# Performance work log

Hardware: AMD Instinct MI355X
Metric: run time of the kernel (lower is better)

The kernel has to match this reference:

```python
import jax, jax.numpy as jnp
import numpy as np

B, S, D, H, L, V, FFM = 4, 2048, 512, 8, 6, 8000, 4
HD = D // H
FF = FFM * D


def setup_inputs() -> dict:
    key = jax.random.key(0)
    ks = jax.random.split(key, 12)
    sc = 0.02
    return {
        "tokens": jax.random.randint(ks[0], (B, S), 0, V),
        "embed": jax.random.normal(ks[1], (V, D), jnp.float32) * sc,
        "wq": jax.random.normal(ks[2], (L, D, D), jnp.float32) * sc,
        "wk": jax.random.normal(ks[3], (L, D, D), jnp.float32) * sc,
        "wv": jax.random.normal(ks[4], (L, D, D), jnp.float32) * sc,
        "wo": jax.random.normal(ks[5], (L, D, D), jnp.float32) * sc,
        "bo": jnp.zeros((L, D), jnp.float32),
        "w1": jax.random.normal(ks[6], (L, D, FF), jnp.float32) * sc,
        "b1": jnp.zeros((L, FF), jnp.float32),
        "w2": jax.random.normal(ks[7], (L, FF, D), jnp.float32) * sc,
        "b2": jnp.zeros((L, D), jnp.float32),
        "ln_g": jnp.ones((L, D), jnp.float32),
        "ln_b": jnp.zeros((L, D), jnp.float32),
        "lnf_g": jnp.ones((D,), jnp.float32),
        "lnf_b": jnp.zeros((D,), jnp.float32),
        "w_out": jax.random.normal(ks[8], (D, V), jnp.float32) * sc,
        "b_out": jnp.zeros((V,), jnp.float32),
    }


def _layernorm(x, g, b, eps=1e-5):
    m = jnp.mean(x, -1, keepdims=True)
    v = jnp.var(x, -1, keepdims=True)
    return (x - m) * jax.lax.rsqrt(v + eps) * g + b


def _pos_encoding():
    pos = jnp.arange(S, dtype=jnp.float32)[:, None]
    div = jnp.exp(jnp.arange(0, D, 2, dtype=jnp.float32) * (-np.log(10000.0) / D))
    pe = jnp.zeros((S, D), jnp.float32)
    pe = pe.at[:, 0::2].set(jnp.sin(pos * div))
    pe = pe.at[:, 1::2].set(jnp.cos(pos * div))
    return pe


def _forward(tokens, embed, wq, wk, wv, wo, bo, w1, b1, w2, b2, ln_g, ln_b,
             lnf_g, lnf_b, w_out, b_out):
    x = embed[tokens] + _pos_encoding()[None]  # [B,S,D]
    causal = jnp.tril(jnp.ones((S, S), bool))
    neg_inf = jnp.float32(-jnp.inf)
    # NOTE: original scales scores by 1/sqrt(n_embd) (key.weight.size(-1) == D)
    inv_scale = 1.0 / jnp.sqrt(jnp.float32(D))

    def block(x, p):
        pwq, pwk, pwv, pwo, pbo, pw1, pb1, pw2, pb2, g, b = p
        # attention sublayer (same LayerNorm params used for both sublayers,
        # matching the repo's reuse of add_and_norm_1)
        h = _layernorm(x, g, b)
        q = (h @ pwq).reshape(B, S, H, HD)
        k = (h @ pwk).reshape(B, S, H, HD)
        v = (h @ pwv).reshape(B, S, H, HD)
        scores = jnp.einsum('bqhd,bkhd->bhqk', q, k) * inv_scale
        scores = jnp.where(causal, scores, neg_inf)
        att = jax.nn.softmax(scores, axis=-1)
        o = jnp.einsum('bhqk,bkhd->bqhd', att, v).reshape(B, S, D)
        x = x + o @ pwo + pbo
        # FFN sublayer
        h2 = _layernorm(x, g, b)
        x = x + jax.nn.relu(h2 @ pw1 + pb1) @ pw2 + pb2
        return x, None

    params = (wq, wk, wv, wo, bo, w1, b1, w2, b2, ln_g, ln_b)
    x, _ = jax.lax.scan(block, x, params)
    x = _layernorm(x, lnf_g, lnf_b)
    logits = x @ w_out + b_out  # [B,S,V]
    return logits


def reference(tokens, embed, wq, wk, wv, wo, bo, w1, b1, w2, b2, ln_g, ln_b,
              lnf_g, lnf_b, w_out, b_out):
    return _forward(tokens, embed, wq, wk, wv, wo, bo, w1, b1, w2, b2,
                    ln_g, ln_b, lnf_g, lnf_b, w_out, b_out)
```

## Files before the change

kernel.cpp:

```cpp
#include <hip/hip_runtime.h>

#define Bsz 4
#define Ssz 2048
#define Dsz 512
#define Hsz 8
#define Lsz 6
#define Vsz 8000
#define FFsz 2048
#define Msz (Bsz*Ssz)
#define VszPad 8064

typedef unsigned short u16;
typedef unsigned int u32;
typedef __attribute__((ext_vector_type(8))) short bf16x8;
typedef __attribute__((ext_vector_type(4))) float f32x4;
typedef __attribute__((ext_vector_type(16))) float f32x16;
typedef __attribute__((ext_vector_type(4))) u32 u32x4;

__device__ __forceinline__ u16 f2b(float f) {
    union { float f; unsigned u; } x; x.f = f;
    return (u16)((x.u + 0x7fffu + ((x.u >> 16) & 1u)) >> 16);
}

#define GLOAD_LDS16(g, l) __builtin_amdgcn_global_load_lds( \
    (const __attribute__((address_space(1))) u32*)(g), \
    (__attribute__((address_space(3))) u32*)(l), 16, 0, 0)

__global__ __launch_bounds__(256) void embed_kernel(const int* __restrict__ tokens,
                                                    const float* __restrict__ embed,
                                                    float* __restrict__ x) {
    int idx = blockIdx.x * 256 + threadIdx.x;
    int row = idx >> 8, p = idx & 255;
    int tok = tokens[row];
    int s = row & (Ssz - 1);
    float div = __expf((float)p * (-9.210340371976184f / 256.f));
    float ang = (float)s * div;
    float2 e = ((const float2*)(embed + (size_t)tok * Dsz))[p];
    float2 o;
    o.x = e.x + sinf(ang);
    o.y = e.y + cosf(ang);
    ((float2*)(x + (size_t)row * Dsz))[p] = o;
}

__global__ __launch_bounds__(256) void ln_kernel(const float* __restrict__ x,
                                                 const float* __restrict__ g,
                                                 const float* __restrict__ bta,
                                                 u16* __restrict__ out) {
    int wave = threadIdx.x >> 6, lane = threadIdx.x & 63;
    int row = blockIdx.x * 4 + wave;
    const float4* xr = (const float4*)(x + (size_t)row * Dsz);
    float4 a = xr[lane * 2], c = xr[lane * 2 + 1];
    float vals[8] = {a.x, a.y, a.z, a.w, c.x, c.y, c.z, c.w};
    float s = 0.f;
    #pragma unroll
    for (int i = 0; i < 8; ++i) s += vals[i];
    #pragma unroll
    for (int o = 32; o; o >>= 1) s += __shfl_xor(s, o);
    float mean = s * (1.f / 512.f);
    float sq = 0.f;
    #pragma unroll
    for (int i = 0; i < 8; ++i) { float d = vals[i] - mean; sq += d * d; }
    #pragma unroll
    for (int o = 32; o; o >>= 1) sq += __shfl_xor(sq, o);
    float rstd = rsqrtf(sq * (1.f / 512.f) + 1e-5f);
    int base = lane * 8;
    bf16x8 rv;
    #pragma unroll
    for (int i = 0; i < 8; ++i)
        rv[i] = (short)f2b((vals[i] - mean) * rstd * g[base + i] + bta[base + i]);
    *(bf16x8*)(out + (size_t)row * Dsz + base) = rv;
}

__global__ __launch_bounds__(256) void tconv_kernel(const float* __restrict__ src,
                                                    u16* __restrict__ dst,
                                                    int R, int C,
                                                    size_t sstride, size_t dstride) {
    __shared__ float tile[32][33];
    const float* s = src + blockIdx.z * sstride;
    u16* d = dst + blockIdx.z * dstride;
    int c0 = blockIdx.x * 32, r0 = blockIdx.y * 32;
    int tx = threadIdx.x & 31, ty = threadIdx.x >> 5;
    #pragma unroll
    for (int i = 0; i < 32; i += 8)
        tile[ty + i][tx] = s[(size_t)(r0 + ty + i) * C + c0 + tx];
    __syncthreads();
    #pragma unroll
    for (int i = 0; i < 32; i += 8)
        d[(size_t)(c0 + ty + i) * R + r0 + tx] = f2b(tile[tx][ty + i]);
}

__global__ __launch_bounds__(256) void vtrans_kernel(const u16* __restrict__ qkv,
                                                     u16* __restrict__ vT) {
    __shared__ u16 tile[32][33];
    int bh = blockIdx.z, b = bh >> 3, hh = bh & 7;
    int s0 = blockIdx.x * 32, d0 = blockIdx.y * 32;
    int tx = threadIdx.x & 31, ty = threadIdx.x >> 5;
    #pragma unroll
    for (int i = 0; i < 32; i += 8)
        tile[ty + i][tx] = qkv[(size_t)(b * Ssz + s0 + ty + i) * 1536 + 1024 + hh * 64 + d0 + tx];
    __syncthreads();
    #pragma unroll
    for (int i = 0; i < 32; i += 8)
        vT[((size_t)bh * 64 + d0 + ty + i) * Ssz + s0 + tx] = tile[tx][ty + i];
}

template<bool BIAS, bool RES, bool RELU, bool OF32, bool OBF16>
__global__ __launch_bounds__(256) void gemm_kernel(const u16* __restrict__ A,
                                                   const u16* __restrict__ BT,
                                                   const float* __restrict__ bias,
                                                   const float* __restrict__ res,
                                                   float* __restrict__ outf,
                                                   u16* __restrict__ outb,
                                                   int M, int N, int K) {
    __shared__ u16 As[128 * 64];
    __shared__ u16 Bs[128 * 64];
    int tid = threadIdx.x;
    int wave = tid >> 6, lane = tid & 63;
    int wm = wave >> 1, wn = wave & 1;
    int nwg = gridDim.x * gridDim.y;
    int bid = blockIdx.y * gridDim.x + blockIdx.x;
    int swz = (bid & 7) * (nwg >> 3) + (bid >> 3);
    int m0 = (swz / gridDim.x) * 128, n0 = (swz % gridDim.x) * 128;
    int lr = lane & 15, lg = lane >> 4;
    int srow = lane >> 3;
    int scol = (lane & 7) * 8;
    f32x4 acc[4][4] = {};
    for (int k0 = 0; k0 < K; k0 += 64) {
        #pragma unroll
        for (int i = 0; i < 4; ++i) {
            int chunk = wave * 4 + i;
            int r = chunk * 8 + srow;
            GLOAD_LDS16(A + (size_t)(m0 + r) * K + k0 + scol, &As[chunk * 512]);
            GLOAD_LDS16(BT + (size_t)(n0 + r) * K + k0 + scol, &Bs[chunk * 512]);
        }
        __syncthreads();
        #pragma unroll
        for (int kk = 0; kk < 2; ++kk) {
            bf16x8 af[4], bfr[4];
            #pragma unroll
            for (int m = 0; m < 4; ++m)
                af[m] = *(const bf16x8*)(As + (wm * 64 + m * 16 + lr) * 64 + kk * 32 + lg * 8);
            #pragma unroll
            for (int n = 0; n < 4; ++n)
                bfr[n] = *(const bf16x8*)(Bs + (wn * 64 + n * 16 + lr) * 64 + kk * 32 + lg * 8);
            #pragma unroll
            for (int m = 0; m < 4; ++m)
                #pragma unroll
                for (int n = 0; n < 4; ++n)
                    acc[m][n] = __builtin_amdgcn_mfma_f32_16x16x32_bf16(af[m], bfr[n], acc[m][n], 0, 0, 0);
        }
        __syncthreads();
    }
    #pragma unroll
    for (int m = 0; m < 4; ++m) {
        int row = m0 + wm * 64 + m * 16 + lg * 4;
        #pragma unroll
        for (int n = 0; n < 4; ++n) {
            int col = n0 + wn * 64 + n * 16 + lr;
            if (col < N) {
                float bv = BIAS ? bias[col] : 0.f;
                #pragma unroll
                for (int j = 0; j < 4; ++j) {
                    float v = acc[m][n][j] + bv;
                    if (RES) v += res[(size_t)(row + j) * N + col];
                    if (RELU) v = fmaxf(v, 0.f);
                    if (OF32) outf[(size_t)(row + j) * N + col] = v;
                    if (OBF16) outb[(size_t)(row + j) * N + col] = f2b(v);
                }
            }
        }
    }
}

__global__ __launch_bounds__(256) void flash2_kernel(const u16* __restrict__ qkv,
                                                     const u16* __restrict__ vT,
                                                     u16* __restrict__ o) {
    __shared__ u16 Ks[64 * 64];
    __shared__ u16 Vs[64 * 64];
    int qt = (gridDim.x - 1) - blockIdx.x;
    int bh = blockIdx.y, b = bh >> 3, hh = bh & 7;
    int tid = threadIdx.x, wave = tid >> 6, lane = tid & 63;
    int l31 = lane & 31, h5 = lane >> 5;
    int q0 = qt * 128;
    int qw0 = q0 + wave * 32;
    int qg = qw0 + l31;
    const float cs = 0.044194173824159216f;

    bf16x8 qf[4];
    {
        const u16* qrow = qkv + (size_t)(b * Ssz + qg) * 1536 + hh * 64;
        #pragma unroll
        for (int cb = 0; cb < 4; ++cb)
            qf[cb] = *(const bf16x8*)(qrow + cb * 16 + h5 * 8);
    }
    f32x16 Oa0 = {}, Oa1 = {};
    float m_run = -1e30f, l_run = 0.f;
    int sr = tid >> 3;
    int sc = (tid & 7) * 8;
    int nt = 2 * qt + 2;

    for (int kt = 0; kt < nt; ++kt) {
        #pragma unroll
        for (int p = 0; p < 2; ++p) {
            int r = p * 32 + sr;
            bf16x8 kv_ = *(const bf16x8*)(qkv + (size_t)(b * Ssz + kt * 64 + r) * 1536 + 512 + hh * 64 + sc);
            bf16x8 vv  = *(const bf16x8*)(vT + ((size_t)bh * 64 + r) * Ssz + kt * 64 + sc);
            int byte = (r * 128 + sc * 2) ^ ((r & 7) << 4);
            *(bf16x8*)((char*)Ks + byte) = kv_;
            *(bf16x8*)((char*)Vs + byte) = vv;
        }
        __syncthreads();
        if (kt * 64 <= qw0 + 31) {
            f32x16 st[2] = {};
            #pragma unroll
            for (int mt = 0; mt < 2; ++mt)
                #pragma unroll
                for (int cb = 0; cb < 4; ++cb) {
                    int r = mt * 32 + l31;
                    int byte = (r * 128 + (cb * 16 + h5 * 8) * 2) ^ ((r & 7) << 4);
                    bf16x8 kf = *(const bf16x8*)((char*)Ks + byte);
                    st[mt] = __builtin_amdgcn_mfma_f32_32x32x16_bf16(kf, qf[cb], st[mt], 0, 0, 0);
                }
            bool dtile = (kt * 64 + 63 > qw0);
            float pmax = -1e30f;
            #pragma unroll
            for (int mt = 0; mt < 2; ++mt)
                #pragma unroll
                for (int r = 0; r < 16; ++r) {
                    float v = st[mt][r];
                    if (dtile) {
                        int kglob = kt * 64 + mt * 32 + (r & 3) + 8 * (r >> 2) + 4 * h5;
                        if (kglob > qg) v = -1e30f;
                    }
                    st[mt][r] = v;
                    pmax = fmaxf(pmax, v);
                }
            pmax = fmaxf(pmax, __shfl_xor(pmax, 32));
            if (!__all(pmax - m_run <= 181.019336f)) {
                float mn = fmaxf(m_run, pmax);
                float al = __expf((m_run - mn) * cs);
                l_run *= al;
                #pragma unroll
                for (int r = 0; r < 16; ++r) {
                    int qloc = (r & 3) + 8 * (r >> 2) + 4 * h5;
                    float alr = __shfl(al, qloc);
                    Oa0[r] *= alr; Oa1[r] *= alr;
                }
                m_run = mn;
            }
            float ls = 0.f;
            u32 pk[2][8];
            #pragma unroll
            for (int mt = 0; mt < 2; ++mt)
                #pragma unroll
                for (int w = 0; w < 8; ++w) {
                    float p0 = __expf((st[mt][2 * w]     - m_run) * cs);
                    float p1 = __expf((st[mt][2 * w + 1] - m_run) * cs);
                    ls += p0 + p1;
                    pk[mt][w] = (u32)f2b(p0) | ((u32)f2b(p1) << 16);
                }
            l_run += ls + __shfl_xor(ls, 32);
            #pragma unroll
            for (int mt = 0; mt < 2; ++mt) {
                u32 pko[8];
                #pragma unroll
                for (int w = 0; w < 8; ++w)
                    pko[w] = __shfl_xor(pk[mt][w], 32);
                #pragma unroll
                for (int kbl = 0; kbl < 2; ++kbl) {
                    int kb = mt * 2 + kbl;
                    u32x4 aw;
                    #pragma unroll
                    for (int w = 0; w < 4; ++w) {
                        int widx = 4 * kbl + 2 * h5 + (w & 1);
                        bool own = (w < 2) != (h5 == 1);
                        aw[w] = own ? pk[mt][widx] : pko[widx];
                    }
                    bf16x8 af = __builtin_bit_cast(bf16x8, aw);
                    #pragma unroll
                    for (int dt = 0; dt < 2; ++dt) {
                        int r = dt * 32 + l31;
                        int byte = (r * 128 + (kb * 16 + h5 * 8) * 2) ^ ((r & 7) << 4);
                        bf16x8 vf = *(const bf16x8*)((char*)Vs + byte);
                        if (dt == 0) Oa0 = __builtin_amdgcn_mfma_f32_32x32x16_bf16(af, vf, Oa0, 0, 0, 0);
                        else         Oa1 = __builtin_amdgcn_mfma_f32_32x32x16_bf16(af, vf, Oa1, 0, 0, 0);
                    }
                }
            }
        }
        __syncthreads();
    }
    float rln = 1.f / l_run;
    u16* obase = o + (size_t)(b * Ssz) * Dsz + hh * 64;
    #pragma unroll
    for (int r = 0; r < 16; ++r) {
        int qloc = (r & 3) + 8 * (r >> 2) + 4 * h5;
        float s = __shfl(rln, qloc);
        u16* orow = obase + (size_t)(qw0 + qloc) * Dsz + l31;
        orow[0]  = f2b(Oa0[r] * s);
        orow[32] = f2b(Oa1[r] * s);
    }
}

extern "C" void kernel_launch(void* const* d_in, const int* in_sizes, int n_in,
                              void* d_out, int out_size, void* d_ws, size_t ws_size,
                              hipStream_t stream) {
    (void)in_sizes; (void)n_in; (void)out_size; (void)ws_size;
    const int*   tokens = (const int*)d_in[0];
    const float* embed  = (const float*)d_in[1];
    const float* wq     = (const float*)d_in[2];
    const float* wk     = (const float*)d_in[3];
    const float* wv     = (const float*)d_in[4];
    const float* wo     = (const float*)d_in[5];
    const float* bo     = (const float*)d_in[6];
    const float* w1     = (const float*)d_in[7];
    const float* b1     = (const float*)d_in[8];
    const float* w2     = (const float*)d_in[9];
    const float* b2     = (const float*)d_in[10];
    const float* ln_g   = (const float*)d_in[11];
    const float* ln_b   = (const float*)d_in[12];
    const float* lnf_g  = (const float*)d_in[13];
    const float* lnf_b  = (const float*)d_in[14];
    const float* w_out  = (const float*)d_in[15];
    const float* b_out  = (const float*)d_in[16];
    float* out = (float*)d_out;

    char* ws = (char*)d_ws;
    size_t off = 0;
    auto alloc = [&](size_t bytes) {
        void* p = ws + off;
        off += (bytes + 255) & ~(size_t)255;
        return p;
    };
    float* x     = (float*)alloc((size_t)Msz * Dsz * 4);
    u16*   h     = (u16*)alloc((size_t)Msz * Dsz * 2);
    u16*   qkv   = (u16*)alloc((size_t)Msz * 1536 * 2);
    u16*   vT    = (u16*)alloc((size_t)Bsz * Hsz * 64 * Ssz * 2);
    u16*   ob    = (u16*)alloc((size_t)Msz * Dsz * 2);
    u16*   ffh   = (u16*)alloc((size_t)Msz * FFsz * 2);
    u16*   wqkvT = (u16*)alloc((size_t)Lsz * 3 * Dsz * Dsz * 2);
    u16*   woT   = (u16*)alloc((size_t)Lsz * Dsz * Dsz * 2);
    u16*   w1T   = (u16*)alloc((size_t)Lsz * FFsz * Dsz * 2);
    u16*   w2T   = (u16*)alloc((size_t)Lsz * Dsz * FFsz * 2);
    u16*   w_outT= (u16*)alloc((size_t)VszPad * Dsz * 2);

    dim3 tb(256);
    size_t dd = (size_t)Dsz * Dsz;
    hipMemsetAsync(w_outT + (size_t)Vsz * Dsz, 0, (size_t)(VszPad - Vsz) * Dsz * 2, stream);
    tconv_kernel<<<dim3(16, 16, Lsz), tb, 0, stream>>>(wq, wqkvT + 0 * dd, Dsz, Dsz, dd, 3 * dd);
    tconv_kernel<<<dim3(16, 16, Lsz), tb, 0, stream>>>(wk, wqkvT + 1 * dd, Dsz, Dsz, dd, 3 * dd);
    tconv_kernel<<<dim3(16, 16, Lsz), tb, 0, stream>>>(wv, wqkvT + 2 * dd, Dsz, Dsz, dd, 3 * dd);
    tconv_kernel<<<dim3(16, 16, Lsz), tb, 0, stream>>>(wo, woT, Dsz, Dsz, dd, dd);
    tconv_kernel<<<dim3(64, 16, Lsz), tb, 0, stream>>>(w1, w1T, Dsz, FFsz, (size_t)Dsz * FFsz, (size_t)FFsz * Dsz);
    tconv_kernel<<<dim3(16, 64, Lsz), tb, 0, stream>>>(w2, w2T, FFsz, Dsz, (size_t)FFsz * Dsz, (size_t)Dsz * FFsz);
    tconv_kernel<<<dim3(250, 16, 1), tb, 0, stream>>>(w_out, w_outT, Dsz, Vsz, 0, 0);

    embed_kernel<<<Msz * 256 / 256, tb, 0, stream>>>(tokens, embed, x);

    for (int l = 0; l < Lsz; ++l) {
        ln_kernel<<<Msz / 4, tb, 0, stream>>>(x, ln_g + l * Dsz, ln_b + l * Dsz, h);
        gemm_kernel<false, false, false, false, true><<<dim3(12, Msz / 128), tb, 0, stream>>>(
            h, wqkvT + (size_t)l * 3 * dd, nullptr, nullptr, nullptr, qkv, Msz, 1536, Dsz);
        vtrans_kernel<<<dim3(Ssz / 32, 2, Bsz * Hsz), tb, 0, stream>>>(qkv, vT);
        flash2_kernel<<<dim3(Ssz / 128, Bsz * Hsz), tb, 0, stream>>>(qkv, vT, ob);
        gemm_kernel<true, true, false, true, false><<<dim3(4, Msz / 128), tb, 0, stream>>>(
            ob, woT + (size_t)l * dd, bo + l * Dsz, x, x, nullptr, Msz, Dsz, Dsz);
        ln_kernel<<<Msz / 4, tb, 0, stream>>>(x, ln_g + l * Dsz, ln_b + l * Dsz, h);
        gemm_kernel<true, false, true, false, true><<<dim3(16, Msz / 128), tb, 0, stream>>>(
            h, w1T + (size_t)l * FFsz * Dsz, b1 + l * FFsz, nullptr, nullptr, ffh, Msz, FFsz, Dsz);
        gemm_kernel<true, true, false, true, false><<<dim3(4, Msz / 128), tb, 0, stream>>>(
            ffh, w2T + (size_t)l * Dsz * FFsz, b2 + l * Dsz, x, x, nullptr, Msz, Dsz, FFsz);
    }
    ln_kernel<<<Msz / 4, tb, 0, stream>>>(x, lnf_g, lnf_b, h);
    gemm_kernel<true, false, false, true, false><<<dim3(63, Msz / 128), tb, 0, stream>>>(
        h, w_outT, b_out, nullptr, out, nullptr, Msz, Vsz, Dsz);
}
```

Measured before the change: 1.837 ms.

## Replace shared-memory flash attention with single-wave blocks reading K/V directly

The 256-thread flash attention kernel that staged K and V tiles through LDS with block-wide barriers is replaced by 64-thread single-wave blocks. Each block reads K and V fragments straight from global memory into MFMA operands and handles a balanced pair of causal query groups (g and 63-g). Block indices are remapped so the heads of one batch land on the same XCD for L2 locality, and s_setprio raises priority around the MFMA sections. This drops LDS traffic and __syncthreads, but each wave now loads K/V redundantly from global memory or cache with no reuse across waves.

```diff
diff --git a/kernel.cpp b/kernel.cpp
--- a/kernel.cpp
+++ b/kernel.cpp
@@ -172,123 +172,102 @@
     }
 }
 
-__global__ __launch_bounds__(256) void flash2_kernel(const u16* __restrict__ qkv,
-                                                     const u16* __restrict__ vT,
-                                                     u16* __restrict__ o) {
-    __shared__ u16 Ks[64 * 64];
-    __shared__ u16 Vs[64 * 64];
-    int qt = (gridDim.x - 1) - blockIdx.x;
-    int bh = blockIdx.y, b = bh >> 3, hh = bh & 7;
-    int tid = threadIdx.x, wave = tid >> 6, lane = tid & 63;
-    int l31 = lane & 31, h5 = lane >> 5;
-    int q0 = qt * 128;
-    int qw0 = q0 + wave * 32;
-    int qg = qw0 + l31;
+__device__ __forceinline__ void flash_group(const u16* __restrict__ qkv,
+                                            const u16* __restrict__ vT,
+                                            u16* __restrict__ o,
+                                            int b, int hh, int bh, int g,
+                                            int l31, int h5) {
     const float cs = 0.044194173824159216f;
-
+    int qg = g * 32 + l31;
+    const u16* qrow = qkv + (size_t)(b * Ssz + qg) * 1536 + hh * 64;
     bf16x8 qf[4];
-    {
-        const u16* qrow = qkv + (size_t)(b * Ssz + qg) * 1536 + hh * 64;
-        #pragma unroll
-        for (int cb = 0; cb < 4; ++cb)
-            qf[cb] = *(const bf16x8*)(qrow + cb * 16 + h5 * 8);
-    }
+    #pragma unroll
+    for (int cb = 0; cb < 4; ++cb)
+        qf[cb] = *(const bf16x8*)(qrow + cb * 16 + h5 * 8);
     f32x16 Oa0 = {}, Oa1 = {};
     float m_run = -1e30f, l_run = 0.f;
-    int sr = tid >> 3;
-    int sc = (tid & 7) * 8;
-    int nt = 2 * qt + 2;
-
+    int nt = (g >> 1) + 1;
+    const u16* kbase = qkv + (size_t)(b * Ssz) * 1536 + 512 + hh * 64;
+    const u16* vbase = vT + (size_t)bh * 64 * Ssz;
     for (int kt = 0; kt < nt; ++kt) {
-        #pragma unroll
-        for (int p = 0; p < 2; ++p) {
-            int r = p * 32 + sr;
-            bf16x8 kv_ = *(const bf16x8*)(qkv + (size_t)(b * Ssz + kt * 64 + r) * 1536 + 512 + hh * 64 + sc);
-            bf16x8 vv  = *(const bf16x8*)(vT + ((size_t)bh * 64 + r) * Ssz + kt * 64 + sc);
-            int byte = (r * 128 + sc * 2) ^ ((r & 7) << 4);
-            *(bf16x8*)((char*)Ks + byte) = kv_;
-            *(bf16x8*)((char*)Vs + byte) = vv;
-        }
-        __syncthreads();
-        if (kt * 64 <= qw0 + 31) {
-            f32x16 st[2] = {};
-            #pragma unroll
-            for (int mt = 0; mt < 2; ++mt)
+        f32x16 st[2] = {};
+        __builtin_amdgcn_s_setprio(1);
+        #pragma unroll
+        for (int mt = 0; mt < 2; ++mt) {
+            const u16* kr = kbase + (size_t)(kt * 64 + mt * 32 + l31) * 1536;
+            #pragma unroll
+            for (int cb = 0; cb < 4; ++cb) {
+                bf16x8 kf = *(const bf16x8*)(kr + cb * 16 + h5 * 8);
+                st[mt] = __builtin_amdgcn_mfma_f32_32x32x16_bf16(kf, qf[cb], st[mt], 0, 0, 0);
+            }
+        }
+        __builtin_amdgcn_s_setprio(0);
+        bool dtile = (kt == nt - 1);
+        float pmax = -1e30f;
+        #pragma unroll
+        for (int mt = 0; mt < 2; ++mt)
+            #pragma unroll
+            for (int r = 0; r < 16; ++r) {
+                float v = st[mt][r];
+                if (dtile) {
+                    int kglob = kt * 64 + mt * 32 + (r & 3) + 8 * (r >> 2) + 4 * h5;
+                    if (kglob > qg) v = -1e30f;
+                }
+                st[mt][r] = v;
+                pmax = fmaxf(pmax, v);
+            }
+        pmax = fmaxf(pmax, __shfl_xor(pmax, 32));
+        if (!__all(pmax - m_run <= 181.019336f)) {
+            float mn = fmaxf(m_run, pmax);
+            float al = __expf((m_run - mn) * cs);
+            l_run *= al;
+            #pragma unroll
+            for (int r = 0; r < 16; ++r) {
+                int qloc = (r & 3) + 8 * (r >> 2) + 4 * h5;
+                float alr = __shfl(al, qloc);
+                Oa0[r] *= alr; Oa1[r] *= alr;
+            }
+            m_run = mn;
+        }
+        float ls = 0.f;
+        u32 pk[2][8];
+        #pragma unroll
+        for (int mt = 0; mt < 2; ++mt)
+            #pragma unroll
+            for (int w = 0; w < 8; ++w) {
+                float p0 = __expf((st[mt][2 * w]     - m_run) * cs);
+                float p1 = __expf((st[mt][2 * w + 1] - m_run) * cs);
+                ls += p0 + p1;
+                pk[mt][w] = (u32)f2b(p0) | ((u32)f2b(p1) << 16);
+            }
+        l_run += ls + __shfl_xor(ls, 32);
+        __builtin_amdgcn_s_setprio(1);
+        #pragma unroll
+        for (int mt = 0; mt < 2; ++mt) {
+            u32 pko[8];
+            #pragma unroll
+            for (int w = 0; w < 8; ++w)
+                pko[w] = __shfl_xor(pk[mt][w], 32);
+            #pragma unroll
+            for (int kbl = 0; kbl < 2; ++kbl) {
+                int kb = mt * 2 + kbl;
+                u32x4 aw;
                 #pragma unroll
-                for (int cb = 0; cb < 4; ++cb) {
-                    int r = mt * 32 + l31;
-                    int byte = (r * 128 + (cb * 16 + h5 * 8) * 2) ^ ((r & 7) << 4);
-                    bf16x8 kf = *(const bf16x8*)((char*)Ks + byte);
-                    st[mt] = __builtin_amdgcn_mfma_f32_32x32x16_bf16(kf, qf[cb], st[mt], 0, 0, 0);
+                for (int w = 0; w < 4; ++w) {
+                    int widx = 4 * kbl + 2 * h5 + (w & 1);
+                    bool own = (w < 2) != (h5 == 1);
+                    aw[w] = own ? pk[mt][widx] : pko[widx];
                 }
-            bool dtile = (kt * 64 + 63 > qw0);
-            float pmax = -1e30f;
-            #pragma unroll
-            for (int mt = 0; mt < 2; ++mt)
+                bf16x8 af = __builtin_bit_cast(bf16x8, aw);
                 #pragma unroll
-                for (int r = 0; r < 16; ++r) {
-                    float v = st[mt][r];
-                    if (dtile) {
-                        int kglob = kt * 64 + mt * 32 + (r & 3) + 8 * (r >> 2) + 4 * h5;
-                        if (kglob > qg) v = -1e30f;
-                    }
-                    st[mt][r] = v;
-                    pmax = fmaxf(pmax, v);
+                for (int dt = 0; dt < 2; ++dt) {
+                    bf16x8 vf = *(const bf16x8*)(vbase + (size_t)(dt * 32 + l31) * Ssz + kt * 64 + kb * 16 + h5 * 8);
+                    if (dt == 0) Oa0 = __builtin_amdgcn_mfma_f32_32x32x16_bf16(af, vf, Oa0, 0, 0, 0);
+                    else         Oa1 = __builtin_amdgcn_mfma_f32_32x32x16_bf16(af, vf, Oa1, 0, 0, 0);
                 }
-            pmax = fmaxf(pmax, __shfl_xor(pmax, 32));
-            if (!__all(pmax - m_run <= 181.019336f)) {
-                float mn = fmaxf(m_run, pmax);
-                float al = __expf((m_run - mn) * cs);
-                l_run *= al;
-                #pragma unroll
-                for (int r = 0; r < 16; ++r) {
-                    int qloc = (r & 3) + 8 * (r >> 2) + 4 * h5;
-                    float alr = __shfl(al, qloc);
-                    Oa0[r] *= alr; Oa1[r] *= alr;
-                }
-                m_run = mn;
-            }
-            float ls = 0.f;
-            u32 pk[2][8];
-            #pragma unroll
-            for (int mt = 0; mt < 2; ++mt)
-                #pragma unroll
-                for (int w = 0; w < 8; ++w) {
-                    float p0 = __expf((st[mt][2 * w]     - m_run) * cs);
-                    float p1 = __expf((st[mt][2 * w + 1] - m_run) * cs);
-                    ls += p0 + p1;
-                    pk[mt][w] = (u32)f2b(p0) | ((u32)f2b(p1) << 16);
-                }
-            l_run += ls + __shfl_xor(ls, 32);
-            #pragma unroll
-            for (int mt = 0; mt < 2; ++mt) {
-                u32 pko[8];
-                #pragma unroll
-                for (int w = 0; w < 8; ++w)
-                    pko[w] = __shfl_xor(pk[mt][w], 32);
-                #pragma unroll
-                for (int kbl = 0; kbl < 2; ++kbl) {
-                    int kb = mt * 2 + kbl;
-                    u32x4 aw;
-                    #pragma unroll
-                    for (int w = 0; w < 4; ++w) {
-                        int widx = 4 * kbl + 2 * h5 + (w & 1);
-                        bool own = (w < 2) != (h5 == 1);
-                        aw[w] = own ? pk[mt][widx] : pko[widx];
-                    }
-                    bf16x8 af = __builtin_bit_cast(bf16x8, aw);
-                    #pragma unroll
-                    for (int dt = 0; dt < 2; ++dt) {
-                        int r = dt * 32 + l31;
-                        int byte = (r * 128 + (kb * 16 + h5 * 8) * 2) ^ ((r & 7) << 4);
-                        bf16x8 vf = *(const bf16x8*)((char*)Vs + byte);
-                        if (dt == 0) Oa0 = __builtin_amdgcn_mfma_f32_32x32x16_bf16(af, vf, Oa0, 0, 0, 0);
-                        else         Oa1 = __builtin_amdgcn_mfma_f32_32x32x16_bf16(af, vf, Oa1, 0, 0, 0);
-                    }
-                }
-            }
-        }
-        __syncthreads();
+            }
+        }
+        __builtin_amdgcn_s_setprio(0);
     }
     float rln = 1.f / l_run;
     u16* obase = o + (size_t)(b * Ssz) * Dsz + hh * 64;
@@ -296,10 +275,23 @@
     for (int r = 0; r < 16; ++r) {
         int qloc = (r & 3) + 8 * (r >> 2) + 4 * h5;
         float s = __shfl(rln, qloc);
-        u16* orow = obase + (size_t)(qw0 + qloc) * Dsz + l31;
+        u16* orow = obase + (size_t)(g * 32 + qloc) * Dsz + l31;
         orow[0]  = f2b(Oa0[r] * s);
         orow[32] = f2b(Oa1[r] * s);
     }
+}
+
+__global__ __launch_bounds__(64) void flash3_kernel(const u16* __restrict__ qkv,
+                                                    const u16* __restrict__ vT,
+                                                    u16* __restrict__ o) {
+    int d = blockIdx.x;
+    int xcd = d & 7, j = d >> 3;
+    int bh = xcd * 4 + (j & 3);
+    int pair = j >> 2;
+    int b = bh >> 3, hh = bh & 7;
+    int l31 = threadIdx.x & 31, h5 = (threadIdx.x & 63) >> 5;
+    flash_group(qkv, vT, o, b, hh, bh, 63 - pair, l31, h5);
+    flash_group(qkv, vT, o, b, hh, bh, pair, l31, h5);
 }
 
 extern "C" void kernel_launch(void* const* d_in, const int* in_sizes, int n_in,
@@ -362,7 +354,7 @@
         gemm_kernel<false, false, false, false, true><<<dim3(12, Msz / 128), tb, 0, stream>>>(
             h, wqkvT + (size_t)l * 3 * dd, nullptr, nullptr, nullptr, qkv, Msz, 1536, Dsz);
         vtrans_kernel<<<dim3(Ssz / 32, 2, Bsz * Hsz), tb, 0, stream>>>(qkv, vT);
-        flash2_kernel<<<dim3(Ssz / 128, Bsz * Hsz), tb, 0, stream>>>(qkv, vT, ob);
+        flash3_kernel<<<dim3(1024), dim3(64), 0, stream>>>(qkv, vT, ob);
         gemm_kernel<true, true, false, true, false><<<dim3(4, Msz / 128), tb, 0, stream>>>(
             ob, woT + (size_t)l * dd, bo + l * Dsz, x, x, nullptr, Msz, Dsz, Dsz);
         ln_kernel<<<Msz / 4, tb, 0, stream>>>(x, ln_g + l * Dsz, ln_b + l * Dsz, h);
```

After: 1.852 ms. Within noise of the previous version (+0.8%).
